# Optimization experiments

Hardware: AMD Instinct MI355X
Metric: run time of the kernel (lower is better)

Reference implementation:

```python
import jax, jax.numpy as jnp
import numpy as np

B, IN, OUT, BR = 64, 8192, 2048, 4
VTH = 0.5
_SQRT_2PI = float(np.sqrt(2.0 * np.pi))


def _gauss(x, mu, sigma):
    return jnp.exp(-((x - mu) ** 2) / (2.0 * sigma ** 2)) / _SQRT_2PI / sigma


@jax.custom_vjp
def act_fun(x):
    return (x > 0.0).astype(x.dtype)


def _act_fwd(x):
    return act_fun(x), x


def _act_bwd(x, g):
    lens, scale, hight, gamma = 0.5, 6.0, 0.15, 0.5
    temp = (_gauss(x, 0.0, lens) * (1.0 + hight)
            - _gauss(x, lens, scale * lens) * hight
            - _gauss(x, -lens, scale * lens) * hight)
    return (g * temp * gamma,)


act_fun.defvjp(_act_fwd, _act_bwd)


def setup_inputs() -> dict:
    key = jax.random.key(0)
    ks = jax.random.split(key, 8)
    fan_in = IN
    bound = 1.0 / np.sqrt(fan_in)
    return {
        "input_spike": jax.random.uniform(ks[0], (B, IN), dtype=jnp.float32),
        "mem": jax.random.uniform(ks[1], (B, OUT), dtype=jnp.float32),
        "spike": jax.random.uniform(ks[2], (B, OUT), dtype=jnp.float32),
        "d_input": jnp.zeros((B, OUT, BR), dtype=jnp.float32),
        "v_th": jnp.ones((B, OUT), dtype=jnp.float32) * VTH,
        "W": jax.random.uniform(ks[3], (OUT * BR, IN), minval=-bound, maxval=bound, dtype=jnp.float32),
        "b": jax.random.uniform(ks[4], (OUT * BR,), minval=-bound, maxval=bound, dtype=jnp.float32),
        "tau_m": jax.random.uniform(ks[5], (OUT,), minval=0.0, maxval=4.0, dtype=jnp.float32),
        "tau_n": jax.random.uniform(ks[6], (OUT, BR), minval=0.0, maxval=4.0, dtype=jnp.float32),
    }


def reference(input_spike, mem, spike, d_input, v_th, W, b, tau_m, tau_n):
    R_m = 1.0
    batch = input_spike.shape[0]
    out_dim, branch = tau_n.shape
    in_dim = W.shape[1]  # padded input size
    chunk = in_dim // branch
    # pad input to in_dim (pad == 0 for these dims, kept for generality)
    pad = in_dim - input_spike.shape[1]
    k = jnp.pad(input_spike.astype(jnp.float32), ((0, 0), (0, pad)))
    # block-masked linear: mask keeps, for neuron o / branch j, only column block j.
    # Equivalent to taking the diagonal blocks of W reshaped [out, branch, branch, chunk].
    W_diag = jnp.einsum("obbc->obc", W.reshape(out_dim, branch, branch, chunk))
    y = jnp.einsum("obc,nbc->nob", W_diag, k.reshape(batch, branch, chunk))
    y = y + b.reshape(out_dim, branch)  # [B, out, branch]
    # per-branch dendritic decay
    beta = jax.nn.sigmoid(tau_n)
    d_new = beta * d_input + (1.0 - beta) * y
    l_input = d_new.sum(axis=2)  # [B, out]
    # LIF with soft reset
    alpha = jax.nn.sigmoid(tau_m)
    mem_new = mem * alpha + (1.0 - alpha) * R_m * l_input - v_th * spike
    spike_new = act_fun(mem_new - v_th)
    return mem_new, spike_new
```

## Files before the change

### kernel.cpp

```cpp
#include <hip/hip_runtime.h>
#include <math.h>

#define BATCH   64
#define IN_DIM  8192
#define OUT_DIM 2048
#define BRANCH  4
#define CHUNK   2048
#define KT      128
#define NT      16

typedef __attribute__((ext_vector_type(8))) short short8;
typedef __attribute__((ext_vector_type(4))) short short4v;
typedef __attribute__((ext_vector_type(4))) float f32x4;

__device__ __forceinline__ float sigmoidf_(float x) {
    return 1.0f / (1.0f + expf(-x));
}

__device__ __forceinline__ unsigned rne_bf16(float f) {
    unsigned u = __float_as_uint(f);
    return (u + 0x7fffu + ((u >> 16) & 1u)) >> 16;
}

__global__ __launch_bounds__(256) void prep_x(const float* __restrict__ X,
                                              short8* __restrict__ Xfh,
                                              short8* __restrict__ Xfl) {
    const int gid = blockIdx.x * 256 + threadIdx.x;
    const int l  = gid & 63;
    const int kk = (gid >> 6) & 63;
    const int s  = (gid >> 12) & 3;
    const int j  = gid >> 14;
    const int n  = s * 16 + (l & 15);
    const int k0 = kk * 32 + ((l >> 4) << 3);
    const float* p = X + (size_t)n * IN_DIM + j * CHUNK + k0;
    const f32x4 a = *(const f32x4*)p;
    const f32x4 c = *(const f32x4*)(p + 4);
    float v[8] = {a[0], a[1], a[2], a[3], c[0], c[1], c[2], c[3]};
    short8 h, lo;
#pragma unroll
    for (int e = 0; e < 8; ++e) {
        unsigned hb = rne_bf16(v[e]);
        float fh = __uint_as_float(hb << 16);
        unsigned lb = rne_bf16(v[e] - fh);
        h[e]  = (short)hb;
        lo[e] = (short)lb;
    }
    Xfh[gid] = h;
    Xfl[gid] = lo;
}

__device__ __forceinline__ void stage_store(char* Wh, char* Wl, const f32x4* wr,
                                            int wbyte0, int swz, int kq) {
#pragma unroll
    for (int i = 0; i < 4; ++i) {
        unsigned hb[4], lb[4];
#pragma unroll
        for (int e = 0; e < 4; ++e) {
            float f = wr[i][e];
            unsigned h = rne_bf16(f);
            float fh = __uint_as_float(h << 16);
            unsigned l = rne_bf16(f - fh);
            hb[e] = h; lb[e] = l;
        }
        short4v vh = { (short)hb[0], (short)hb[1], (short)hb[2], (short)hb[3] };
        short4v vl = { (short)lb[0], (short)lb[1], (short)lb[2], (short)lb[3] };
        const int kb   = (kq << 5) + (i << 3);
        const int byte = wbyte0 + (kb ^ swz);
        *(short4v*)(Wh + byte) = vh;
        *(short4v*)(Wl + byte) = vl;
    }
}

__global__ __launch_bounds__(256) void dend_gemm(const short8* __restrict__ Xfh,
                                                 const short8* __restrict__ Xfl,
                                                 const float*  __restrict__ W,
                                                 float* __restrict__ Y) {
    __shared__ __align__(16) char WhL[2][32 * 256];
    __shared__ __align__(16) char WlL[2][32 * 256];
    __shared__ float Ys[32][65];

    const int t    = threadIdx.x;
    const int bid  = blockIdx.x;
    const int j    = bid & 3;
    const int o0   = (bid >> 2) << 5;
    const int lane = t & 63;
    const int wv   = t >> 6;

    const int ri  = t >> 3;
    const int kq  = t & 7;
    const float* wsrc = W + (size_t)((o0 + ri) * 4 + j) * IN_DIM + j * CHUNK + kq * 16;
    const int wbyte0 = ri << 8;
    const int swz    = (ri & 15) << 4;

    const short8* pAh = Xfh + (j * 4 + wv) * 4096 + lane;
    const short8* pAl = Xfl + (j * 4 + wv) * 4096 + lane;

    const int o_l   = lane & 15;
    const int bswz  = o_l << 4;
    const int kgrp  = (lane >> 4) << 4;
    const int b0row = o_l << 8;
    const int b1row = (o_l + 16) << 8;

    f32x4 acc0 = {0.f, 0.f, 0.f, 0.f};
    f32x4 acc1 = {0.f, 0.f, 0.f, 0.f};

    f32x4  wr[4];
    short8 Ah0[4], Al0[4], Ah1[4], Al1[4];

#pragma unroll
    for (int i = 0; i < 4; ++i)
        wr[i] = *(const f32x4*)(wsrc + i * 4);
    stage_store(WhL[0], WlL[0], wr, wbyte0, swz, kq);
#pragma unroll
    for (int i = 0; i < 4; ++i)
        wr[i] = *(const f32x4*)(wsrc + KT + i * 4);
#pragma unroll
    for (int i = 0; i < 4; ++i) { Ah0[i] = pAh[i * 64];       Al0[i] = pAl[i * 64]; }
#pragma unroll
    for (int i = 0; i < 4; ++i) { Ah1[i] = pAh[(4 + i) * 64]; Al1[i] = pAl[(4 + i) * 64]; }
    __syncthreads();

#define BODY(kt, AH, AL)                                                            \
  {                                                                                 \
    if ((kt) + 1 < NT)                                                              \
        stage_store(WhL[((kt) + 1) & 1], WlL[((kt) + 1) & 1], wr, wbyte0, swz, kq); \
    if ((kt) + 2 < NT) {                                                            \
        _Pragma("unroll")                                                           \
        for (int i = 0; i < 4; ++i)                                                 \
            wr[i] = *(const f32x4*)(wsrc + ((kt) + 2) * KT + i * 4);                \
    }                                                                               \
    _Pragma("unroll")                                                               \
    for (int st = 0; st < 4; ++st) {                                                \
        const int off = ((st << 6) + kgrp) ^ bswz;                                  \
        short8 bh0 = *(const short8*)(&WhL[(kt) & 1][b0row + off]);                 \
        short8 bl0 = *(const short8*)(&WlL[(kt) & 1][b0row + off]);                 \
        short8 bh1 = *(const short8*)(&WhL[(kt) & 1][b1row + off]);                 \
        short8 bl1 = *(const short8*)(&WlL[(kt) & 1][b1row + off]);                 \
        acc0 = __builtin_amdgcn_mfma_f32_16x16x32_bf16(AH[st], bh0, acc0, 0, 0, 0); \
        acc1 = __builtin_amdgcn_mfma_f32_16x16x32_bf16(AH[st], bh1, acc1, 0, 0, 0); \
        acc0 = __builtin_amdgcn_mfma_f32_16x16x32_bf16(AL[st], bh0, acc0, 0, 0, 0); \
        acc1 = __builtin_amdgcn_mfma_f32_16x16x32_bf16(AL[st], bh1, acc1, 0, 0, 0); \
        acc0 = __builtin_amdgcn_mfma_f32_16x16x32_bf16(AH[st], bl0, acc0, 0, 0, 0); \
        acc1 = __builtin_amdgcn_mfma_f32_16x16x32_bf16(AH[st], bl1, acc1, 0, 0, 0); \
    }                                                                               \
    if ((kt) + 2 < NT) {                                                            \
        _Pragma("unroll")                                                           \
        for (int i = 0; i < 4; ++i) {                                               \
            AH[i] = pAh[(((kt) + 2) * 4 + i) * 64];                                 \
            AL[i] = pAl[(((kt) + 2) * 4 + i) * 64];                                 \
        }                                                                           \
    }                                                                               \
    __syncthreads();                                                                \
  }

#pragma unroll 1
    for (int kt = 0; kt < NT; kt += 2) {
        BODY(kt,     Ah0, Al0)
        BODY(kt + 1, Ah1, Al1)
    }
#undef BODY

    {
        const int rb = (wv << 4) + ((lane >> 4) << 2);
#pragma unroll
        for (int r = 0; r < 4; ++r) {
            Ys[o_l][rb + r]      = acc0[r];
            Ys[o_l + 16][rb + r] = acc1[r];
        }
    }
    __syncthreads();
#pragma unroll
    for (int p = 0; p < 8; ++p) {
        const int e  = t + (p << 8);
        const int oo = e & 31;
        const int n  = e >> 5;
        Y[(size_t)((n << 2) + j) * OUT_DIM + o0 + oo] = Ys[oo][n];
    }
}

__global__ __launch_bounds__(256) void lif_pointwise(
    const float* __restrict__ Y,
    const float* __restrict__ mem,
    const float* __restrict__ spike,
    const float* __restrict__ d_input,
    const float* __restrict__ v_th,
    const float* __restrict__ b,
    const float* __restrict__ tau_m,
    const float* __restrict__ tau_n,
    float* __restrict__ out)
{
    const int idx = blockIdx.x * 256 + threadIdx.x;
    const int o   = idx & (OUT_DIM - 1);
    const int n   = idx >> 11;

    const float4 tn = ((const float4*)tau_n)[o];
    const float4 bb = ((const float4*)b)[o];
    const float4 di = ((const float4*)d_input)[idx];

    const size_t ybase = (size_t)(n * BRANCH) * OUT_DIM + o;
    const float y0 = Y[ybase];
    const float y1 = Y[ybase + OUT_DIM];
    const float y2 = Y[ybase + 2 * OUT_DIM];
    const float y3 = Y[ybase + 3 * OUT_DIM];

    float l = 0.0f;
    { const float bt = sigmoidf_(tn.x); l += bt * di.x + (1.0f - bt) * (y0 + bb.x); }
    { const float bt = sigmoidf_(tn.y); l += bt * di.y + (1.0f - bt) * (y1 + bb.y); }
    { const float bt = sigmoidf_(tn.z); l += bt * di.z + (1.0f - bt) * (y2 + bb.z); }
    { const float bt = sigmoidf_(tn.w); l += bt * di.w + (1.0f - bt) * (y3 + bb.w); }

    const float alpha = sigmoidf_(tau_m[o]);
    const float vt    = v_th[idx];
    const float m     = mem[idx] * alpha + (1.0f - alpha) * l - vt * spike[idx];

    out[idx] = m;
    out[BATCH * OUT_DIM + idx] = (m - vt) > 0.0f ? 1.0f : 0.0f;
}

extern "C" void kernel_launch(void* const* d_in, const int* in_sizes, int n_in,
                              void* d_out, int out_size, void* d_ws, size_t ws_size,
                              hipStream_t stream) {
    const float* X     = (const float*)d_in[0];
    const float* mem   = (const float*)d_in[1];
    const float* spike = (const float*)d_in[2];
    const float* dinp  = (const float*)d_in[3];
    const float* vth   = (const float*)d_in[4];
    const float* W     = (const float*)d_in[5];
    const float* b     = (const float*)d_in[6];
    const float* tm    = (const float*)d_in[7];
    const float* tn    = (const float*)d_in[8];
    float* out = (float*)d_out;

    short8* Xfh = (short8*)d_ws;
    short8* Xfl = (short8*)((char*)d_ws + (1u << 20));
    float*  Yw  = (float*)((char*)d_ws + (2u << 20));

    prep_x<<<256, 256, 0, stream>>>(X, Xfh, Xfl);
    dend_gemm<<<256, 256, 0, stream>>>(Xfh, Xfl, W, Yw);
    lif_pointwise<<<512, 256, 0, stream>>>(Yw, mem, spike, dinp, vth, b, tm, tn, out);
}
```

Baseline: 31.74 us.

## Split K across eight waves, load W directly into registers, reduce via LDS

The GEMM kernel now uses 512 threads per block. Each of the eight waves owns one K slice and computes the full 64x32 output tile, so it reads and splits W straight from global memory into MFMA operand registers with nontemporal loads. This drops the double-buffered LDS staging of W and the per-step block barriers. Partial sums from the eight waves are combined through a 64KB LDS buffer at the end. The cost is more accumulator registers, a large LDS footprint that can limit occupancy, and an extra reduction pass.

```diff
diff --git a/kernel.cpp b/kernel.cpp
--- a/kernel.cpp
+++ b/kernel.cpp
@@ -6,11 +6,10 @@
 #define OUT_DIM 2048
 #define BRANCH  4
 #define CHUNK   2048
-#define KT      128
-#define NT      16
+#define KSPLIT  8
+#define KSTEPS  8
 
 typedef __attribute__((ext_vector_type(8))) short short8;
-typedef __attribute__((ext_vector_type(4))) short short4v;
 typedef __attribute__((ext_vector_type(4))) float f32x4;
 
 __device__ __forceinline__ float sigmoidf_(float x) {
@@ -49,133 +48,115 @@
     Xfl[gid] = lo;
 }
 
-__device__ __forceinline__ void stage_store(char* Wh, char* Wl, const f32x4* wr,
-                                            int wbyte0, int swz, int kq) {
-#pragma unroll
-    for (int i = 0; i < 4; ++i) {
-        unsigned hb[4], lb[4];
-#pragma unroll
-        for (int e = 0; e < 4; ++e) {
-            float f = wr[i][e];
-            unsigned h = rne_bf16(f);
-            float fh = __uint_as_float(h << 16);
-            unsigned l = rne_bf16(f - fh);
-            hb[e] = h; lb[e] = l;
-        }
-        short4v vh = { (short)hb[0], (short)hb[1], (short)hb[2], (short)hb[3] };
-        short4v vl = { (short)lb[0], (short)lb[1], (short)lb[2], (short)lb[3] };
-        const int kb   = (kq << 5) + (i << 3);
-        const int byte = wbyte0 + (kb ^ swz);
-        *(short4v*)(Wh + byte) = vh;
-        *(short4v*)(Wl + byte) = vl;
-    }
-}
-
-__global__ __launch_bounds__(256) void dend_gemm(const short8* __restrict__ Xfh,
+__device__ __forceinline__ void split8(const f32x4 a, const f32x4 b,
+                                       short8& h, short8& lo) {
+    float v[8] = {a[0], a[1], a[2], a[3], b[0], b[1], b[2], b[3]};
+#pragma unroll
+    for (int e = 0; e < 8; ++e) {
+        unsigned hb = rne_bf16(v[e]);
+        float fh = __uint_as_float(hb << 16);
+        unsigned lb = rne_bf16(v[e] - fh);
+        h[e]  = (short)hb;
+        lo[e] = (short)lb;
+    }
+}
+
+__global__ __launch_bounds__(512) void dend_gemm(const short8* __restrict__ Xfh,
                                                  const short8* __restrict__ Xfl,
                                                  const float*  __restrict__ W,
                                                  float* __restrict__ Y) {
-    __shared__ __align__(16) char WhL[2][32 * 256];
-    __shared__ __align__(16) char WlL[2][32 * 256];
-    __shared__ float Ys[32][65];
+    __shared__ float Ylds[8 * 2048];
 
     const int t    = threadIdx.x;
+    const int lane = t & 63;
+    const int w    = t >> 6;
     const int bid  = blockIdx.x;
     const int j    = bid & 3;
     const int o0   = (bid >> 2) << 5;
-    const int lane = t & 63;
-    const int wv   = t >> 6;
-
-    const int ri  = t >> 3;
-    const int kq  = t & 7;
-    const float* wsrc = W + (size_t)((o0 + ri) * 4 + j) * IN_DIM + j * CHUNK + kq * 16;
-    const int wbyte0 = ri << 8;
-    const int swz    = (ri & 15) << 4;
-
-    const short8* pAh = Xfh + (j * 4 + wv) * 4096 + lane;
-    const short8* pAl = Xfl + (j * 4 + wv) * 4096 + lane;
-
-    const int o_l   = lane & 15;
-    const int bswz  = o_l << 4;
-    const int kgrp  = (lane >> 4) << 4;
-    const int b0row = o_l << 8;
-    const int b1row = (o_l + 16) << 8;
-
-    f32x4 acc0 = {0.f, 0.f, 0.f, 0.f};
-    f32x4 acc1 = {0.f, 0.f, 0.f, 0.f};
-
-    f32x4  wr[4];
-    short8 Ah0[4], Al0[4], Ah1[4], Al1[4];
-
-#pragma unroll
-    for (int i = 0; i < 4; ++i)
-        wr[i] = *(const f32x4*)(wsrc + i * 4);
-    stage_store(WhL[0], WlL[0], wr, wbyte0, swz, kq);
-#pragma unroll
-    for (int i = 0; i < 4; ++i)
-        wr[i] = *(const f32x4*)(wsrc + KT + i * 4);
-#pragma unroll
-    for (int i = 0; i < 4; ++i) { Ah0[i] = pAh[i * 64];       Al0[i] = pAl[i * 64]; }
-#pragma unroll
-    for (int i = 0; i < 4; ++i) { Ah1[i] = pAh[(4 + i) * 64]; Al1[i] = pAl[(4 + i) * 64]; }
+    const int o_l  = lane & 15;
+    const int q    = lane >> 4;
+
+    const float* wp0 = W + (size_t)((o0 + o_l) * 4 + j) * IN_DIM
+                         + j * CHUNK + w * 256 + q * 8;
+    const float* wp1 = wp0 + (size_t)64 * IN_DIM;
+
+    const short8* pAh = Xfh + j * 16384 + w * 512 + lane;
+    const short8* pAl = Xfl + j * 16384 + w * 512 + lane;
+
+    f32x4 acc[4][2];
+#pragma unroll
+    for (int s = 0; s < 4; ++s) { acc[s][0] = (f32x4)0.f; acc[s][1] = (f32x4)0.f; }
+
+    f32x4  Wr[2][2][2];
+    short8 Ah[2][4], Al[2][4];
+
+#pragma unroll
+    for (int h = 0; h < 2; ++h) {
+        Wr[0][0][h] = __builtin_nontemporal_load((const f32x4*)(wp0) + h);
+        Wr[0][1][h] = __builtin_nontemporal_load((const f32x4*)(wp1) + h);
+        Wr[1][0][h] = __builtin_nontemporal_load((const f32x4*)(wp0 + 32) + h);
+        Wr[1][1][h] = __builtin_nontemporal_load((const f32x4*)(wp1 + 32) + h);
+    }
+#pragma unroll
+    for (int s = 0; s < 4; ++s) {
+        Ah[0][s] = pAh[s * 4096];
+        Al[0][s] = pAl[s * 4096];
+    }
+
+#pragma unroll
+    for (int s = 0; s < KSTEPS; ++s) {
+        const int cur = s & 1;
+        const int nxt = cur ^ 1;
+
+        short8 bh0, bl0, bh1, bl1;
+        split8(Wr[cur][0][0], Wr[cur][0][1], bh0, bl0);
+        split8(Wr[cur][1][0], Wr[cur][1][1], bh1, bl1);
+
+        if (s + 2 < KSTEPS) {
+#pragma unroll
+            for (int h = 0; h < 2; ++h) {
+                Wr[cur][0][h] = __builtin_nontemporal_load((const f32x4*)(wp0 + (s + 2) * 32) + h);
+                Wr[cur][1][h] = __builtin_nontemporal_load((const f32x4*)(wp1 + (s + 2) * 32) + h);
+            }
+        }
+        if (s + 1 < KSTEPS) {
+#pragma unroll
+            for (int st = 0; st < 4; ++st) {
+                Ah[nxt][st] = pAh[st * 4096 + (s + 1) * 64];
+                Al[nxt][st] = pAl[st * 4096 + (s + 1) * 64];
+            }
+        }
+
+#pragma unroll
+        for (int st = 0; st < 4; ++st) {
+            acc[st][0] = __builtin_amdgcn_mfma_f32_16x16x32_bf16(Ah[cur][st], bh0, acc[st][0], 0, 0, 0);
+            acc[st][1] = __builtin_amdgcn_mfma_f32_16x16x32_bf16(Ah[cur][st], bh1, acc[st][1], 0, 0, 0);
+            acc[st][0] = __builtin_amdgcn_mfma_f32_16x16x32_bf16(Al[cur][st], bh0, acc[st][0], 0, 0, 0);
+            acc[st][1] = __builtin_amdgcn_mfma_f32_16x16x32_bf16(Al[cur][st], bh1, acc[st][1], 0, 0, 0);
+            acc[st][0] = __builtin_amdgcn_mfma_f32_16x16x32_bf16(Ah[cur][st], bl0, acc[st][0], 0, 0, 0);
+            acc[st][1] = __builtin_amdgcn_mfma_f32_16x16x32_bf16(Ah[cur][st], bl1, acc[st][1], 0, 0, 0);
+        }
+    }
+
+#pragma unroll
+    for (int st = 0; st < 4; ++st)
+#pragma unroll
+        for (int g = 0; g < 2; ++g)
+#pragma unroll
+            for (int r = 0; r < 4; ++r)
+                Ylds[w * 2048 + (st * 16 + q * 4 + r) * 32 + g * 16 + o_l] = acc[st][g][r];
+
     __syncthreads();
 
-#define BODY(kt, AH, AL)                                                            \
-  {                                                                                 \
-    if ((kt) + 1 < NT)                                                              \
-        stage_store(WhL[((kt) + 1) & 1], WlL[((kt) + 1) & 1], wr, wbyte0, swz, kq); \
-    if ((kt) + 2 < NT) {                                                            \
-        _Pragma("unroll")                                                           \
-        for (int i = 0; i < 4; ++i)                                                 \
-            wr[i] = *(const f32x4*)(wsrc + ((kt) + 2) * KT + i * 4);                \
-    }                                                                               \
-    _Pragma("unroll")                                                               \
-    for (int st = 0; st < 4; ++st) {                                                \
-        const int off = ((st << 6) + kgrp) ^ bswz;                                  \
-        short8 bh0 = *(const short8*)(&WhL[(kt) & 1][b0row + off]);                 \
-        short8 bl0 = *(const short8*)(&WlL[(kt) & 1][b0row + off]);                 \
-        short8 bh1 = *(const short8*)(&WhL[(kt) & 1][b1row + off]);                 \
-        short8 bl1 = *(const short8*)(&WlL[(kt) & 1][b1row + off]);                 \
-        acc0 = __builtin_amdgcn_mfma_f32_16x16x32_bf16(AH[st], bh0, acc0, 0, 0, 0); \
-        acc1 = __builtin_amdgcn_mfma_f32_16x16x32_bf16(AH[st], bh1, acc1, 0, 0, 0); \
-        acc0 = __builtin_amdgcn_mfma_f32_16x16x32_bf16(AL[st], bh0, acc0, 0, 0, 0); \
-        acc1 = __builtin_amdgcn_mfma_f32_16x16x32_bf16(AL[st], bh1, acc1, 0, 0, 0); \
-        acc0 = __builtin_amdgcn_mfma_f32_16x16x32_bf16(AH[st], bl0, acc0, 0, 0, 0); \
-        acc1 = __builtin_amdgcn_mfma_f32_16x16x32_bf16(AH[st], bl1, acc1, 0, 0, 0); \
-    }                                                                               \
-    if ((kt) + 2 < NT) {                                                            \
-        _Pragma("unroll")                                                           \
-        for (int i = 0; i < 4; ++i) {                                               \
-            AH[i] = pAh[(((kt) + 2) * 4 + i) * 64];                                 \
-            AL[i] = pAl[(((kt) + 2) * 4 + i) * 64];                                 \
-        }                                                                           \
-    }                                                                               \
-    __syncthreads();                                                                \
-  }
-
-#pragma unroll 1
-    for (int kt = 0; kt < NT; kt += 2) {
-        BODY(kt,     Ah0, Al0)
-        BODY(kt + 1, Ah1, Al1)
-    }
-#undef BODY
-
-    {
-        const int rb = (wv << 4) + ((lane >> 4) << 2);
-#pragma unroll
-        for (int r = 0; r < 4; ++r) {
-            Ys[o_l][rb + r]      = acc0[r];
-            Ys[o_l + 16][rb + r] = acc1[r];
-        }
-    }
-    __syncthreads();
-#pragma unroll
-    for (int p = 0; p < 8; ++p) {
-        const int e  = t + (p << 8);
-        const int oo = e & 31;
-        const int n  = e >> 5;
-        Y[(size_t)((n << 2) + j) * OUT_DIM + o0 + oo] = Ys[oo][n];
-    }
+    f32x4 v = (f32x4)0.f;
+#pragma unroll
+    for (int w2 = 0; w2 < 8; ++w2) {
+        const f32x4 part = *(const f32x4*)&Ylds[w2 * 2048 + (t << 2)];
+        v += part;
+    }
+    const int n  = t >> 3;
+    const int oo = (t << 2) & 31;
+    *(f32x4*)&Y[(size_t)((n << 2) + j) * OUT_DIM + o0 + oo] = v;
 }
 
 __global__ __launch_bounds__(256) void lif_pointwise(
@@ -236,6 +217,6 @@
     float*  Yw  = (float*)((char*)d_ws + (2u << 20));
 
     prep_x<<<256, 256, 0, stream>>>(X, Xfh, Xfl);
-    dend_gemm<<<256, 256, 0, stream>>>(Xfh, Xfl, W, Yw);
+    dend_gemm<<<256, 512, 0, stream>>>(Xfh, Xfl, W, Yw);
     lif_pointwise<<<512, 256, 0, stream>>>(Yw, mem, spike, dinp, vth, b, tm, tn, out);
 }
```

After: 45.40 us. 43.1% more time.

## Split dendritic GEMM along K into four segments with partial sums

Applied to the files above, without the earlier changes.

The GEMM grid grows from 256 to 1024 blocks by splitting each chunk's K range into four 512-wide segments. Each block writes its own partial Y, and the pointwise kernel sums the four partials. This targets low occupancy and long serial K loops on a GPU with many CUs. It also adds nontemporal W loads, reuses the W LDS buffer for the transpose, and writes Y with vectorized stores. The cost is four times the Y workspace traffic and extra reads in the LIF kernel.

```diff
diff --git a/kernel.cpp b/kernel.cpp
--- a/kernel.cpp
+++ b/kernel.cpp
@@ -6,8 +6,10 @@
 #define OUT_DIM 2048
 #define BRANCH  4
 #define CHUNK   2048
+#define NSEG    4
+#define KSEG    512
 #define KT      128
-#define NT      16
+#define NT      4
 
 typedef __attribute__((ext_vector_type(8))) short short8;
 typedef __attribute__((ext_vector_type(4))) short short4v;
@@ -71,29 +73,30 @@
     }
 }
 
-__global__ __launch_bounds__(256) void dend_gemm(const short8* __restrict__ Xfh,
-                                                 const short8* __restrict__ Xfl,
-                                                 const float*  __restrict__ W,
-                                                 float* __restrict__ Y) {
+__global__ __launch_bounds__(256, 4) void dend_gemm(const short8* __restrict__ Xfh,
+                                                    const short8* __restrict__ Xfl,
+                                                    const float*  __restrict__ W,
+                                                    float* __restrict__ Yp) {
     __shared__ __align__(16) char WhL[2][32 * 256];
     __shared__ __align__(16) char WlL[2][32 * 256];
-    __shared__ float Ys[32][65];
 
     const int t    = threadIdx.x;
     const int bid  = blockIdx.x;
     const int j    = bid & 3;
-    const int o0   = (bid >> 2) << 5;
+    const int o0   = ((bid >> 2) & 63) << 5;
+    const int ks   = bid >> 8;
     const int lane = t & 63;
     const int wv   = t >> 6;
 
     const int ri  = t >> 3;
     const int kq  = t & 7;
-    const float* wsrc = W + (size_t)((o0 + ri) * 4 + j) * IN_DIM + j * CHUNK + kq * 16;
+    const float* wsrc = W + (size_t)((o0 + ri) * 4 + j) * IN_DIM
+                          + j * CHUNK + ks * KSEG + kq * 16;
     const int wbyte0 = ri << 8;
     const int swz    = (ri & 15) << 4;
 
-    const short8* pAh = Xfh + (j * 4 + wv) * 4096 + lane;
-    const short8* pAl = Xfl + (j * 4 + wv) * 4096 + lane;
+    const short8* pAh = Xfh + (j * 4 + wv) * 4096 + ks * 1024 + lane;
+    const short8* pAl = Xfl + (j * 4 + wv) * 4096 + ks * 1024 + lane;
 
     const int o_l   = lane & 15;
     const int bswz  = o_l << 4;
@@ -105,61 +108,53 @@
     f32x4 acc1 = {0.f, 0.f, 0.f, 0.f};
 
     f32x4  wr[4];
-    short8 Ah0[4], Al0[4], Ah1[4], Al1[4];
+    short8 Ah[4], Al[4];
 
 #pragma unroll
     for (int i = 0; i < 4; ++i)
-        wr[i] = *(const f32x4*)(wsrc + i * 4);
+        wr[i] = __builtin_nontemporal_load((const f32x4*)(wsrc + i * 4));
     stage_store(WhL[0], WlL[0], wr, wbyte0, swz, kq);
 #pragma unroll
     for (int i = 0; i < 4; ++i)
-        wr[i] = *(const f32x4*)(wsrc + KT + i * 4);
-#pragma unroll
-    for (int i = 0; i < 4; ++i) { Ah0[i] = pAh[i * 64];       Al0[i] = pAl[i * 64]; }
-#pragma unroll
-    for (int i = 0; i < 4; ++i) { Ah1[i] = pAh[(4 + i) * 64]; Al1[i] = pAl[(4 + i) * 64]; }
+        wr[i] = __builtin_nontemporal_load((const f32x4*)(wsrc + KT + i * 4));
+#pragma unroll
+    for (int i = 0; i < 4; ++i) { Ah[i] = pAh[i * 64]; Al[i] = pAl[i * 64]; }
     __syncthreads();
 
-#define BODY(kt, AH, AL)                                                            \
-  {                                                                                 \
-    if ((kt) + 1 < NT)                                                              \
-        stage_store(WhL[((kt) + 1) & 1], WlL[((kt) + 1) & 1], wr, wbyte0, swz, kq); \
-    if ((kt) + 2 < NT) {                                                            \
-        _Pragma("unroll")                                                           \
-        for (int i = 0; i < 4; ++i)                                                 \
-            wr[i] = *(const f32x4*)(wsrc + ((kt) + 2) * KT + i * 4);                \
-    }                                                                               \
-    _Pragma("unroll")                                                               \
-    for (int st = 0; st < 4; ++st) {                                                \
-        const int off = ((st << 6) + kgrp) ^ bswz;                                  \
-        short8 bh0 = *(const short8*)(&WhL[(kt) & 1][b0row + off]);                 \
-        short8 bl0 = *(const short8*)(&WlL[(kt) & 1][b0row + off]);                 \
-        short8 bh1 = *(const short8*)(&WhL[(kt) & 1][b1row + off]);                 \
-        short8 bl1 = *(const short8*)(&WlL[(kt) & 1][b1row + off]);                 \
-        acc0 = __builtin_amdgcn_mfma_f32_16x16x32_bf16(AH[st], bh0, acc0, 0, 0, 0); \
-        acc1 = __builtin_amdgcn_mfma_f32_16x16x32_bf16(AH[st], bh1, acc1, 0, 0, 0); \
-        acc0 = __builtin_amdgcn_mfma_f32_16x16x32_bf16(AL[st], bh0, acc0, 0, 0, 0); \
-        acc1 = __builtin_amdgcn_mfma_f32_16x16x32_bf16(AL[st], bh1, acc1, 0, 0, 0); \
-        acc0 = __builtin_amdgcn_mfma_f32_16x16x32_bf16(AH[st], bl0, acc0, 0, 0, 0); \
-        acc1 = __builtin_amdgcn_mfma_f32_16x16x32_bf16(AH[st], bl1, acc1, 0, 0, 0); \
-    }                                                                               \
-    if ((kt) + 2 < NT) {                                                            \
-        _Pragma("unroll")                                                           \
-        for (int i = 0; i < 4; ++i) {                                               \
-            AH[i] = pAh[(((kt) + 2) * 4 + i) * 64];                                 \
-            AL[i] = pAl[(((kt) + 2) * 4 + i) * 64];                                 \
-        }                                                                           \
-    }                                                                               \
-    __syncthreads();                                                                \
-  }
-
-#pragma unroll 1
-    for (int kt = 0; kt < NT; kt += 2) {
-        BODY(kt,     Ah0, Al0)
-        BODY(kt + 1, Ah1, Al1)
-    }
-#undef BODY
-
+#pragma unroll
+    for (int kt = 0; kt < NT; ++kt) {
+        if (kt + 1 < NT)
+            stage_store(WhL[(kt + 1) & 1], WlL[(kt + 1) & 1], wr, wbyte0, swz, kq);
+        if (kt + 2 < NT) {
+#pragma unroll
+            for (int i = 0; i < 4; ++i)
+                wr[i] = __builtin_nontemporal_load((const f32x4*)(wsrc + (kt + 2) * KT + i * 4));
+        }
+#pragma unroll
+        for (int st = 0; st < 4; ++st) {
+            const int off = ((st << 6) + kgrp) ^ bswz;
+            short8 bh0 = *(const short8*)(&WhL[kt & 1][b0row + off]);
+            short8 bl0 = *(const short8*)(&WlL[kt & 1][b0row + off]);
+            short8 bh1 = *(const short8*)(&WhL[kt & 1][b1row + off]);
+            short8 bl1 = *(const short8*)(&WlL[kt & 1][b1row + off]);
+            acc0 = __builtin_amdgcn_mfma_f32_16x16x32_bf16(Ah[st], bh0, acc0, 0, 0, 0);
+            acc1 = __builtin_amdgcn_mfma_f32_16x16x32_bf16(Ah[st], bh1, acc1, 0, 0, 0);
+            acc0 = __builtin_amdgcn_mfma_f32_16x16x32_bf16(Al[st], bh0, acc0, 0, 0, 0);
+            acc1 = __builtin_amdgcn_mfma_f32_16x16x32_bf16(Al[st], bh1, acc1, 0, 0, 0);
+            acc0 = __builtin_amdgcn_mfma_f32_16x16x32_bf16(Ah[st], bl0, acc0, 0, 0, 0);
+            acc1 = __builtin_amdgcn_mfma_f32_16x16x32_bf16(Ah[st], bl1, acc1, 0, 0, 0);
+        }
+        if (kt + 1 < NT) {
+#pragma unroll
+            for (int i = 0; i < 4; ++i) {
+                Ah[i] = pAh[((kt + 1) * 4 + i) * 64];
+                Al[i] = pAl[((kt + 1) * 4 + i) * 64];
+            }
+        }
+        __syncthreads();
+    }
+
+    float (*Ys)[66] = (float (*)[66])(&WhL[0][0]);
     {
         const int rb = (wv << 4) + ((lane >> 4) << 2);
 #pragma unroll
@@ -169,17 +164,20 @@
         }
     }
     __syncthreads();
-#pragma unroll
-    for (int p = 0; p < 8; ++p) {
-        const int e  = t + (p << 8);
-        const int oo = e & 31;
-        const int n  = e >> 5;
-        Y[(size_t)((n << 2) + j) * OUT_DIM + o0 + oo] = Ys[oo][n];
+    {
+        const int o4 = (t & 7) << 2;
+        const int n  = t >> 3;
+#pragma unroll
+        for (int h = 0; h < 2; ++h) {
+            const int nn = n + h * 32;
+            f32x4 v = { Ys[o4][nn], Ys[o4 + 1][nn], Ys[o4 + 2][nn], Ys[o4 + 3][nn] };
+            *(f32x4*)&Yp[(size_t)(((ks * 64 + nn) << 2) + j) * OUT_DIM + o0 + o4] = v;
+        }
     }
 }
 
 __global__ __launch_bounds__(256) void lif_pointwise(
-    const float* __restrict__ Y,
+    const float* __restrict__ Yp,
     const float* __restrict__ mem,
     const float* __restrict__ spike,
     const float* __restrict__ d_input,
@@ -197,11 +195,15 @@
     const float4 bb = ((const float4*)b)[o];
     const float4 di = ((const float4*)d_input)[idx];
 
-    const size_t ybase = (size_t)(n * BRANCH) * OUT_DIM + o;
-    const float y0 = Y[ybase];
-    const float y1 = Y[ybase + OUT_DIM];
-    const float y2 = Y[ybase + 2 * OUT_DIM];
-    const float y3 = Y[ybase + 3 * OUT_DIM];
+    float y0 = 0.f, y1 = 0.f, y2 = 0.f, y3 = 0.f;
+#pragma unroll
+    for (int s = 0; s < NSEG; ++s) {
+        const size_t base = (size_t)(((s * BATCH + n) << 2)) * OUT_DIM + o;
+        y0 += Yp[base];
+        y1 += Yp[base + OUT_DIM];
+        y2 += Yp[base + 2 * OUT_DIM];
+        y3 += Yp[base + 3 * OUT_DIM];
+    }
 
     float l = 0.0f;
     { const float bt = sigmoidf_(tn.x); l += bt * di.x + (1.0f - bt) * (y0 + bb.x); }
@@ -233,9 +235,9 @@
 
     short8* Xfh = (short8*)d_ws;
     short8* Xfl = (short8*)((char*)d_ws + (1u << 20));
-    float*  Yw  = (float*)((char*)d_ws + (2u << 20));
+    float*  Yp  = (float*)((char*)d_ws + (2u << 20));
 
     prep_x<<<256, 256, 0, stream>>>(X, Xfh, Xfl);
-    dend_gemm<<<256, 256, 0, stream>>>(Xfh, Xfl, W, Yw);
-    lif_pointwise<<<512, 256, 0, stream>>>(Yw, mem, spike, dinp, vth, b, tm, tn, out);
-}
+    dend_gemm<<<1024, 256, 0, stream>>>(Xfh, Xfl, W, Yp);
+    lif_pointwise<<<512, 256, 0, stream>>>(Yp, mem, spike, dinp, vth, b, tm, tn, out);
+}
```

New measurement: 44.82 us. +41.2%, slower.

## Split GEMM K dimension into two segments and reduce partials in pointwise kernel

Applied to the files above, without the earlier changes.

The dendritic GEMM now splits each branch's 2048-wide K range into two 1024-wide segments, doubling the grid from 256 to 512 blocks, with each block writing partial sums to a separate workspace slice. The LIF pointwise kernel sums the two partials before applying decay and the threshold. The goal is better occupancy across the GPU's compute units, since 256 blocks underfill the device. The cost is extra partial-sum traffic to and from global memory and a changed summation order.

```diff
diff --git a/kernel.cpp b/kernel.cpp
--- a/kernel.cpp
+++ b/kernel.cpp
@@ -6,8 +6,10 @@
 #define OUT_DIM 2048
 #define BRANCH  4
 #define CHUNK   2048
+#define NSEG    2
+#define KSEG    1024
 #define KT      128
-#define NT      16
+#define NT      8
 
 typedef __attribute__((ext_vector_type(8))) short short8;
 typedef __attribute__((ext_vector_type(4))) short short4v;
@@ -74,7 +76,7 @@
 __global__ __launch_bounds__(256) void dend_gemm(const short8* __restrict__ Xfh,
                                                  const short8* __restrict__ Xfl,
                                                  const float*  __restrict__ W,
-                                                 float* __restrict__ Y) {
+                                                 float* __restrict__ Yp) {
     __shared__ __align__(16) char WhL[2][32 * 256];
     __shared__ __align__(16) char WlL[2][32 * 256];
     __shared__ float Ys[32][65];
@@ -82,18 +84,20 @@
     const int t    = threadIdx.x;
     const int bid  = blockIdx.x;
     const int j    = bid & 3;
-    const int o0   = (bid >> 2) << 5;
+    const int o0   = ((bid >> 2) & 63) << 5;
+    const int ks   = bid >> 8;
     const int lane = t & 63;
     const int wv   = t >> 6;
 
     const int ri  = t >> 3;
     const int kq  = t & 7;
-    const float* wsrc = W + (size_t)((o0 + ri) * 4 + j) * IN_DIM + j * CHUNK + kq * 16;
+    const float* wsrc = W + (size_t)((o0 + ri) * 4 + j) * IN_DIM
+                          + j * CHUNK + ks * KSEG + kq * 16;
     const int wbyte0 = ri << 8;
     const int swz    = (ri & 15) << 4;
 
-    const short8* pAh = Xfh + (j * 4 + wv) * 4096 + lane;
-    const short8* pAl = Xfl + (j * 4 + wv) * 4096 + lane;
+    const short8* pAh = Xfh + (j * 4 + wv) * 4096 + ks * 2048 + lane;
+    const short8* pAl = Xfl + (j * 4 + wv) * 4096 + ks * 2048 + lane;
 
     const int o_l   = lane & 15;
     const int bswz  = o_l << 4;
@@ -174,12 +178,12 @@
         const int e  = t + (p << 8);
         const int oo = e & 31;
         const int n  = e >> 5;
-        Y[(size_t)((n << 2) + j) * OUT_DIM + o0 + oo] = Ys[oo][n];
+        Yp[(size_t)(((ks * BATCH + n) << 2) + j) * OUT_DIM + o0 + oo] = Ys[oo][n];
     }
 }
 
 __global__ __launch_bounds__(256) void lif_pointwise(
-    const float* __restrict__ Y,
+    const float* __restrict__ Yp,
     const float* __restrict__ mem,
     const float* __restrict__ spike,
     const float* __restrict__ d_input,
@@ -197,11 +201,15 @@
     const float4 bb = ((const float4*)b)[o];
     const float4 di = ((const float4*)d_input)[idx];
 
-    const size_t ybase = (size_t)(n * BRANCH) * OUT_DIM + o;
-    const float y0 = Y[ybase];
-    const float y1 = Y[ybase + OUT_DIM];
-    const float y2 = Y[ybase + 2 * OUT_DIM];
-    const float y3 = Y[ybase + 3 * OUT_DIM];
+    float y0 = 0.f, y1 = 0.f, y2 = 0.f, y3 = 0.f;
+#pragma unroll
+    for (int s = 0; s < NSEG; ++s) {
+        const size_t base = (size_t)((s * BATCH + n) << 2) * OUT_DIM + o;
+        y0 += Yp[base];
+        y1 += Yp[base + OUT_DIM];
+        y2 += Yp[base + 2 * OUT_DIM];
+        y3 += Yp[base + 3 * OUT_DIM];
+    }
 
     float l = 0.0f;
     { const float bt = sigmoidf_(tn.x); l += bt * di.x + (1.0f - bt) * (y0 + bb.x); }
@@ -233,9 +241,9 @@
 
     short8* Xfh = (short8*)d_ws;
     short8* Xfl = (short8*)((char*)d_ws + (1u << 20));
-    float*  Yw  = (float*)((char*)d_ws + (2u << 20));
+    float*  Yp  = (float*)((char*)d_ws + (2u << 20));
 
     prep_x<<<256, 256, 0, stream>>>(X, Xfh, Xfl);
-    dend_gemm<<<256, 256, 0, stream>>>(Xfh, Xfl, W, Yw);
-    lif_pointwise<<<512, 256, 0, stream>>>(Yw, mem, spike, dinp, vth, b, tm, tn, out);
-}
+    dend_gemm<<<512, 256, 0, stream>>>(Xfh, Xfl, W, Yp);
+    lif_pointwise<<<512, 256, 0, stream>>>(Yp, mem, spike, dinp, vth, b, tm, tn, out);
+}
```

After: 28.16 us. 11.3% less time.
